# Kernel optimization log

Measured on AMD Instinct MI355X. Metric: run time of the kernel, lower is better.

## Reference

```python
import jax, jax.numpy as jnp
import numpy as np

B, H, W, C = 8, 64, 64, 128
BN_EPS = 1e-3  # keras BatchNormalization default epsilon


def setup_inputs() -> dict:
    key = jax.random.key(0)
    ks = jax.random.split(key, 8)
    scale = 1.0 / np.sqrt(C)
    return {
        "x": jax.random.normal(ks[0], (B, H, W, C), dtype=jnp.float32),
        "wq": jax.random.normal(ks[1], (C, C), dtype=jnp.float32) * scale,
        "bq": jnp.zeros((C,), dtype=jnp.float32),
        "wk": jax.random.normal(ks[2], (C, C), dtype=jnp.float32) * scale,
        "bk": jnp.zeros((C,), dtype=jnp.float32),
        "wv": jax.random.normal(ks[3], (C, C), dtype=jnp.float32) * scale,
        "bv": jnp.zeros((C,), dtype=jnp.float32),
        "gamma": jnp.ones((C,), dtype=jnp.float32),
        "beta": jnp.zeros((C,), dtype=jnp.float32),
        "mov_mean": jax.random.normal(ks[4], (C,), dtype=jnp.float32) * 0.1,
        "mov_var": jax.random.uniform(ks[5], (C,), dtype=jnp.float32) * 0.5 + 0.5,
    }


def reference(x, wq, bq, wk, bk, wv, bv, gamma, beta, mov_mean, mov_var):
    b, h, w, c = x.shape
    n = h * w
    # 1x1 convs == per-pixel linear projections
    q = (jnp.einsum('bhwc,cd->bhwd', x, wq) + bq).reshape(b, n, c)
    k = (jnp.einsum('bhwc,cd->bhwd', x, wk) + bk).reshape(b, n, c)
    v = (jnp.einsum('bhwc,cd->bhwd', x, wv) + bv).reshape(b, n, c)
    # full [n, n] attention matrix (as in the original module)
    scores = jnp.einsum('bnc,bmc->bnm', q, k) / jnp.sqrt(jnp.asarray(c, x.dtype))
    attn = jax.nn.softmax(scores, axis=-1)  # dropout is identity in inference
    out = jnp.einsum('bnm,bmc->bnc', attn, v).reshape(b, h, w, c)
    out = out + x  # residual
    # BatchNormalization, inference mode (moving statistics)
    inv = gamma * jax.lax.rsqrt(mov_var + BN_EPS)
    out = out * inv + (beta - mov_mean * inv)
    return out
```

## Files before the change

kernel.cpp:

```cpp
#include <hip/hip_runtime.h>


typedef __attribute__((ext_vector_type(8))) short bf16x8;
typedef __attribute__((ext_vector_type(4))) float f32x4;

__device__ __forceinline__ unsigned short f2bf(float f) {
  unsigned int u = __builtin_bit_cast(unsigned int, f);
  u += 0x7fffu + ((u >> 16) & 1u);
  return (unsigned short)(u >> 16);
}
__device__ __forceinline__ unsigned int pack2(float a, float b) {
  return (unsigned int)f2bf(a) | ((unsigned int)f2bf(b) << 16);
}

#define SCALE_Q (0.08838834764831845f * 1.44269504088896340f)

__global__ void prep_wt(const float* __restrict__ wq, const float* __restrict__ wk,
                        const float* __restrict__ wv, unsigned short* __restrict__ wt) {
  const float* W = (blockIdx.x == 0) ? wq : (blockIdx.x == 1 ? wk : wv);
  const float sc = (blockIdx.x == 0) ? SCALE_Q : 1.0f;
  unsigned short* out = wt + blockIdx.x * 16384;
  int id = blockIdx.y * 256 + threadIdx.x;
  int n  = id >> 5;
  int kb = (id & 31) * 4;
#pragma unroll
  for (int k = 0; k < 4; ++k)
    out[n * 128 + kb + k] = f2bf(W[(kb + k) * 128 + n] * sc);
}

__global__ __launch_bounds__(256) void qkv_fused(
    const float* __restrict__ x, const unsigned short* __restrict__ wt,
    const float* __restrict__ bq, const float* __restrict__ bk, const float* __restrict__ bv,
    unsigned short* __restrict__ Qg, unsigned short* __restrict__ Kg,
    unsigned short* __restrict__ Vtg) {
  __shared__ unsigned short xs[128 * 128];
  __shared__ unsigned short vlds[128 * 136];
  const int t = threadIdx.x;
  const int rowblk = blockIdx.x * 128;

#pragma unroll
  for (int i = 0; i < 16; ++i) {
    int flat = t * 4 + i * 1024;
    int row = flat >> 7, col = flat & 127;
    float4 v = *(const float4*)(x + (size_t)(rowblk + row) * 128 + col);
    unsigned int u0 = pack2(v.x, v.y), u1 = pack2(v.z, v.w);
    int pos = (col >> 3) ^ (row & 15);
    *(uint2*)(xs + row * 128 + pos * 8 + (col & 7)) = make_uint2(u0, u1);
  }
  __syncthreads();

  const int lane = t & 63, wv_ = t >> 6;
  const int lm = lane & 15, quad = lane >> 4;

  bf16x8 a[2][4];
#pragma unroll
  for (int tr = 0; tr < 2; ++tr) {
    int row = wv_ * 32 + tr * 16 + lm;
#pragma unroll
    for (int ks = 0; ks < 4; ++ks)
      a[tr][ks] = __builtin_bit_cast(bf16x8,
          *(const uint4*)(xs + row * 128 + (((ks * 4 + quad) ^ lm) * 8)));
  }

  const f32x4 zero4 = {0.f, 0.f, 0.f, 0.f};
#pragma unroll 1
  for (int p = 0; p < 3; ++p) {
    const unsigned short* w = wt + p * 16384;
    const float* bias = (p == 0) ? bq : (p == 1 ? bk : bv);
    const float bsc = (p == 0) ? SCALE_Q : 1.0f;

    f32x4 acc[2][8];
#pragma unroll
    for (int tr = 0; tr < 2; ++tr)
#pragma unroll
      for (int ct = 0; ct < 8; ++ct) acc[tr][ct] = zero4;

#pragma unroll
    for (int ct = 0; ct < 8; ++ct) {
      int n = ct * 16 + lm;
      const uint4* wp = (const uint4*)(w + n * 128 + quad * 8);
#pragma unroll
      for (int ks = 0; ks < 4; ++ks) {
        bf16x8 bfr = __builtin_bit_cast(bf16x8, wp[ks * 4]);
        acc[0][ct] = __builtin_amdgcn_mfma_f32_16x16x32_bf16(a[0][ks], bfr, acc[0][ct], 0, 0, 0);
        acc[1][ct] = __builtin_amdgcn_mfma_f32_16x16x32_bf16(a[1][ks], bfr, acc[1][ct], 0, 0, 0);
      }
    }

    if (p < 2) {
      unsigned short* og = (p == 0) ? Qg : Kg;
#pragma unroll
      for (int tr = 0; tr < 2; ++tr) {
        int rowb = rowblk + wv_ * 32 + tr * 16 + quad * 4;
#pragma unroll
        for (int ct = 0; ct < 8; ++ct) {
          int c = ct * 16 + lm;
          float bb = bias[c] * bsc;
#pragma unroll
          for (int r = 0; r < 4; ++r)
            og[(size_t)(rowb + r) * 128 + c] = f2bf(acc[tr][ct][r] + bb);
        }
      }
    } else {
#pragma unroll
      for (int tr = 0; tr < 2; ++tr) {
        int key_base = wv_ * 32 + tr * 16 + quad * 4;
#pragma unroll
        for (int ct = 0; ct < 8; ++ct) {
          int c = ct * 16 + lm;
          float bb = bias[c];
          unsigned int u0 = pack2(acc[tr][ct][0] + bb, acc[tr][ct][1] + bb);
          unsigned int u1 = pack2(acc[tr][ct][2] + bb, acc[tr][ct][3] + bb);
          *(uint2*)(vlds + (size_t)c * 136 + key_base) = make_uint2(u0, u1);
        }
      }
      __syncthreads();
      int c2 = t >> 1;
      int ch = (t & 1) * 8;
      int b  = rowblk >> 12;
      int nb0 = rowblk & 4095;
#pragma unroll
      for (int j = 0; j < 8; ++j) {
        uint4 vv = *(const uint4*)(vlds + (size_t)c2 * 136 + (ch + j) * 8);
        *(uint4*)(Vtg + (size_t)b * 524288 + (size_t)c2 * 4096 + nb0 + (ch + j) * 8) = vv;
      }
    }
  }
}

__global__ __launch_bounds__(256, 2) void flash_attn(
    const unsigned short* __restrict__ Qg, const unsigned short* __restrict__ Kg,
    const unsigned short* __restrict__ Vtg, const float* __restrict__ x,
    const float* __restrict__ gamma, const float* __restrict__ beta,
    const float* __restrict__ mmean, const float* __restrict__ mvar,
    float* __restrict__ out) {
  __shared__ uint4 Pb[2048];
  __shared__ float lred[256];

  const int b  = blockIdx.x & 7;
  const int qt = blockIdx.x >> 3;
  const int t = threadIdx.x;
  const int lane = t & 63;
  const int w = t >> 6;
  const int lm = lane & 15, quad = lane >> 4;
  const int q0 = qt * 64;

  const unsigned short* Qb = Qg  + (size_t)b * 524288;
  const unsigned short* Kb = Kg  + (size_t)b * 524288;
  const unsigned short* Vb = Vtg + (size_t)b * 524288;

  bf16x8 qf[4][4];
#pragma unroll
  for (int nt = 0; nt < 4; ++nt) {
    const uint4* qp = (const uint4*)(Qb + (size_t)(q0 + nt * 16 + lm) * 128 + quad * 8);
#pragma unroll
    for (int ks = 0; ks < 4; ++ks) qf[nt][ks] = __builtin_bit_cast(bf16x8, qp[ks * 4]);
  }

  const f32x4 zero4 = {0.f, 0.f, 0.f, 0.f};
  f32x4 o[2][4];
#pragma unroll
  for (int mt = 0; mt < 2; ++mt)
#pragma unroll
    for (int nt = 0; nt < 4; ++nt) o[mt][nt] = zero4;
  float lp[4] = {0.f, 0.f, 0.f, 0.f};

  for (int kt = 0; kt < 32; ++kt) {
    const int key0 = kt * 128;

    bf16x8 kf[2][4], vf[2][4];
#pragma unroll
    for (int mt = 0; mt < 2; ++mt) {
      const uint4* kp = (const uint4*)(Kb + (size_t)(key0 + w * 32 + mt * 16 + lm) * 128 + quad * 8);
      const uint4* vp = (const uint4*)(Vb + (size_t)(w * 32 + mt * 16 + lm) * 4096 + key0 + quad * 8);
#pragma unroll
      for (int ks = 0; ks < 4; ++ks) {
        kf[mt][ks] = __builtin_bit_cast(bf16x8, kp[ks * 4]);
        vf[mt][ks] = __builtin_bit_cast(bf16x8, vp[ks * 4]);
      }
    }

    f32x4 sa[2][4];
#pragma unroll
    for (int mt = 0; mt < 2; ++mt)
#pragma unroll
      for (int nt = 0; nt < 4; ++nt) sa[mt][nt] = zero4;
#pragma unroll
    for (int ks = 0; ks < 4; ++ks)
#pragma unroll
      for (int mt = 0; mt < 2; ++mt)
#pragma unroll
        for (int nt = 0; nt < 4; ++nt)
          sa[mt][nt] = __builtin_amdgcn_mfma_f32_16x16x32_bf16(kf[mt][ks], qf[nt][ks], sa[mt][nt], 0, 0, 0);

    unsigned short* Ps = (unsigned short*)(Pb + (kt & 1) * 1024);
    const int sub = (quad & 1) * 4;
#pragma unroll
    for (int mt = 0; mt < 2; ++mt) {
      int c16 = w * 4 + mt * 2 + (quad >> 1);
      int pos = c16 ^ lm;
#pragma unroll
      for (int nt = 0; nt < 4; ++nt) {
        float e0 = exp2f(sa[mt][nt][0]), e1 = exp2f(sa[mt][nt][1]);
        float e2 = exp2f(sa[mt][nt][2]), e3 = exp2f(sa[mt][nt][3]);
        lp[nt] += (e0 + e1) + (e2 + e3);
        *(uint2*)(Ps + (nt * 16 + lm) * 128 + pos * 8 + sub) =
            make_uint2(pack2(e0, e1), pack2(e2, e3));
      }
    }
    __syncthreads();

    const uint4* Pr = Pb + (kt & 1) * 1024;
#pragma unroll
    for (int nt = 0; nt < 4; ++nt) {
      bf16x8 pf[4];
#pragma unroll
      for (int ks = 0; ks < 4; ++ks)
        pf[ks] = __builtin_bit_cast(bf16x8, Pr[(nt * 16 + lm) * 16 + ((ks * 4 + quad) ^ lm)]);
#pragma unroll
      for (int ks = 0; ks < 4; ++ks)
#pragma unroll
        for (int mt = 0; mt < 2; ++mt)
          o[mt][nt] = __builtin_amdgcn_mfma_f32_16x16x32_bf16(vf[mt][ks], pf[ks], o[mt][nt], 0, 0, 0);
    }
  }

#pragma unroll
  for (int nt = 0; nt < 4; ++nt) {
    lp[nt] += __shfl_xor(lp[nt], 16);
    lp[nt] += __shfl_xor(lp[nt], 32);
  }
  if (quad == 0) {
#pragma unroll
    for (int nt = 0; nt < 4; ++nt) lred[w * 64 + nt * 16 + lm] = lp[nt];
  }
  __syncthreads();
  float rl[4];
#pragma unroll
  for (int nt = 0; nt < 4; ++nt) {
    int q = nt * 16 + lm;
    rl[nt] = 1.0f / ((lred[q] + lred[64 + q]) + (lred[128 + q] + lred[192 + q]));
  }

#pragma unroll
  for (int mt = 0; mt < 2; ++mt) {
    int c0 = w * 32 + mt * 16 + quad * 4;
    float4 gm = *(const float4*)(gamma + c0);
    float4 bt = *(const float4*)(beta + c0);
    float4 mm = *(const float4*)(mmean + c0);
    float4 mv = *(const float4*)(mvar + c0);
    float iv0 = gm.x * rsqrtf(mv.x + 1e-3f), iv1 = gm.y * rsqrtf(mv.y + 1e-3f);
    float iv2 = gm.z * rsqrtf(mv.z + 1e-3f), iv3 = gm.w * rsqrtf(mv.w + 1e-3f);
    float ad0 = bt.x - mm.x * iv0, ad1 = bt.y - mm.y * iv1;
    float ad2 = bt.z - mm.z * iv2, ad3 = bt.w - mm.w * iv3;
#pragma unroll
    for (int nt = 0; nt < 4; ++nt) {
      size_t g = ((size_t)b * 4096 + q0 + nt * 16 + lm) * 128 + c0;
      float4 xr = *(const float4*)(x + g);
      float4 ov;
      ov.x = (o[mt][nt][0] * rl[nt] + xr.x) * iv0 + ad0;
      ov.y = (o[mt][nt][1] * rl[nt] + xr.y) * iv1 + ad1;
      ov.z = (o[mt][nt][2] * rl[nt] + xr.z) * iv2 + ad2;
      ov.w = (o[mt][nt][3] * rl[nt] + xr.w) * iv3 + ad3;
      *(float4*)(out + g) = ov;
    }
  }
}

extern "C" void kernel_launch(void* const* d_in, const int* in_sizes, int n_in,
                              void* d_out, int out_size, void* d_ws, size_t ws_size,
                              hipStream_t stream) {
  const float* x     = (const float*)d_in[0];
  const float* wq    = (const float*)d_in[1];
  const float* bq    = (const float*)d_in[2];
  const float* wk    = (const float*)d_in[3];
  const float* bk    = (const float*)d_in[4];
  const float* wv    = (const float*)d_in[5];
  const float* bv    = (const float*)d_in[6];
  const float* gamma = (const float*)d_in[7];
  const float* beta  = (const float*)d_in[8];
  const float* mmean = (const float*)d_in[9];
  const float* mvar  = (const float*)d_in[10];
  float* out = (float*)d_out;

  unsigned short* wt  = (unsigned short*)d_ws;
  unsigned short* Qg  = wt + 3 * 128 * 128;
  unsigned short* Kg  = Qg + 8 * 4096 * 128;
  unsigned short* Vtg = Kg + 8 * 4096 * 128;

  prep_wt<<<dim3(3, 16), dim3(256), 0, stream>>>(wq, wk, wv, wt);
  qkv_fused<<<dim3(256), dim3(256), 0, stream>>>(x, wt, bq, bk, bv, Qg, Kg, Vtg);
  flash_attn<<<dim3(512), dim3(256), 0, stream>>>(Qg, Kg, Vtg, x, gamma, beta, mmean, mvar, out);
}
```

Before: 233.4 us.

## Prefetch next K tile in attention loop and stage Q/K stores through LDS

The attention loop is restructured to double-buffer the K fragments: the next tile's K is loaded into registers while the current tile is processed, with a manual two-step unroll. This aims to hide global load latency behind the MFMA work. Separately, the QKV projection now stages Q and K outputs through a shared LDS buffer, so global writes become coalesced 16-byte stores instead of scattered 2-byte ones, at the cost of two extra barriers per projection. The extra K registers may lower occupancy under the launch bounds.

```diff
diff --git a/kernel.cpp b/kernel.cpp
--- a/kernel.cpp
+++ b/kernel.cpp
@@ -34,7 +34,7 @@
     unsigned short* __restrict__ Qg, unsigned short* __restrict__ Kg,
     unsigned short* __restrict__ Vtg) {
   __shared__ unsigned short xs[128 * 128];
-  __shared__ unsigned short vlds[128 * 136];
+  __shared__ unsigned short obuf[128 * 136];
   const int t = threadIdx.x;
   const int rowblk = blockIdx.x * 128;
 
@@ -63,6 +63,11 @@
   }
 
   const f32x4 zero4 = {0.f, 0.f, 0.f, 0.f};
+  const int b   = rowblk >> 12;
+  const int nb0 = rowblk & 4095;
+  const int rrow = t >> 1;
+  const int rch  = (t & 1) * 8;
+
 #pragma unroll 1
   for (int p = 0; p < 3; ++p) {
     const unsigned short* w = wt + p * 16384;
@@ -88,19 +93,26 @@
     }
 
     if (p < 2) {
-      unsigned short* og = (p == 0) ? Qg : Kg;
 #pragma unroll
       for (int tr = 0; tr < 2; ++tr) {
-        int rowb = rowblk + wv_ * 32 + tr * 16 + quad * 4;
+        int rowb = wv_ * 32 + tr * 16 + quad * 4;
 #pragma unroll
         for (int ct = 0; ct < 8; ++ct) {
           int c = ct * 16 + lm;
           float bb = bias[c] * bsc;
 #pragma unroll
           for (int r = 0; r < 4; ++r)
-            og[(size_t)(rowb + r) * 128 + c] = f2bf(acc[tr][ct][r] + bb);
+            obuf[(rowb + r) * 136 + c] = f2bf(acc[tr][ct][r] + bb);
         }
       }
+      __syncthreads();
+      unsigned short* og = (p == 0) ? Qg : Kg;
+#pragma unroll
+      for (int j = 0; j < 8; ++j) {
+        uint4 vv = *(const uint4*)(obuf + rrow * 136 + (rch + j) * 8);
+        *(uint4*)(og + (size_t)(rowblk + rrow) * 128 + (rch + j) * 8) = vv;
+      }
+      __syncthreads();
     } else {
 #pragma unroll
       for (int tr = 0; tr < 2; ++tr) {
@@ -111,18 +123,14 @@
           float bb = bias[c];
           unsigned int u0 = pack2(acc[tr][ct][0] + bb, acc[tr][ct][1] + bb);
           unsigned int u1 = pack2(acc[tr][ct][2] + bb, acc[tr][ct][3] + bb);
-          *(uint2*)(vlds + (size_t)c * 136 + key_base) = make_uint2(u0, u1);
+          *(uint2*)(obuf + (size_t)c * 136 + key_base) = make_uint2(u0, u1);
         }
       }
       __syncthreads();
-      int c2 = t >> 1;
-      int ch = (t & 1) * 8;
-      int b  = rowblk >> 12;
-      int nb0 = rowblk & 4095;
 #pragma unroll
       for (int j = 0; j < 8; ++j) {
-        uint4 vv = *(const uint4*)(vlds + (size_t)c2 * 136 + (ch + j) * 8);
-        *(uint4*)(Vtg + (size_t)b * 524288 + (size_t)c2 * 4096 + nb0 + (ch + j) * 8) = vv;
+        uint4 vv = *(const uint4*)(obuf + rrow * 136 + (rch + j) * 8);
+        *(uint4*)(Vtg + (size_t)b * 524288 + (size_t)rrow * 4096 + nb0 + (rch + j) * 8) = vv;
       }
     }
   }
@@ -165,21 +173,28 @@
     for (int nt = 0; nt < 4; ++nt) o[mt][nt] = zero4;
   float lp[4] = {0.f, 0.f, 0.f, 0.f};
 
-  for (int kt = 0; kt < 32; ++kt) {
+  bf16x8 kf0[2][4], kf1[2][4];
+
+  auto loadK = [&](int kt, bf16x8 (&kf)[2][4]) {
     const int key0 = kt * 128;
-
-    bf16x8 kf[2][4], vf[2][4];
 #pragma unroll
     for (int mt = 0; mt < 2; ++mt) {
       const uint4* kp = (const uint4*)(Kb + (size_t)(key0 + w * 32 + mt * 16 + lm) * 128 + quad * 8);
+#pragma unroll
+      for (int ks = 0; ks < 4; ++ks) kf[mt][ks] = __builtin_bit_cast(bf16x8, kp[ks * 4]);
+    }
+  };
+  auto loadV = [&](int kt, bf16x8 (&vf)[2][4]) {
+    const int key0 = kt * 128;
+#pragma unroll
+    for (int mt = 0; mt < 2; ++mt) {
       const uint4* vp = (const uint4*)(Vb + (size_t)(w * 32 + mt * 16 + lm) * 4096 + key0 + quad * 8);
 #pragma unroll
-      for (int ks = 0; ks < 4; ++ks) {
-        kf[mt][ks] = __builtin_bit_cast(bf16x8, kp[ks * 4]);
-        vf[mt][ks] = __builtin_bit_cast(bf16x8, vp[ks * 4]);
-      }
-    }
-
+      for (int ks = 0; ks < 4; ++ks) vf[mt][ks] = __builtin_bit_cast(bf16x8, vp[ks * 4]);
+    }
+  };
+
+  auto body = [&](int kt, bf16x8 (&kf)[2][4], bf16x8 (&vf)[2][4]) {
     f32x4 sa[2][4];
 #pragma unroll
     for (int mt = 0; mt < 2; ++mt)
@@ -222,6 +237,23 @@
 #pragma unroll
         for (int mt = 0; mt < 2; ++mt)
           o[mt][nt] = __builtin_amdgcn_mfma_f32_16x16x32_bf16(vf[mt][ks], pf[ks], o[mt][nt], 0, 0, 0);
+    }
+  };
+
+  loadK(0, kf0);
+#pragma unroll 1
+  for (int kt = 0; kt < 32; kt += 2) {
+    {
+      bf16x8 vf[2][4];
+      loadV(kt, vf);
+      loadK(kt + 1, kf1);
+      body(kt, kf0, vf);
+    }
+    {
+      bf16x8 vf[2][4];
+      loadV(kt + 1, vf);
+      if (kt + 2 < 32) loadK(kt + 2, kf0);
+      body(kt + 1, kf1, vf);
     }
   }
 
```

After: 254.5 us. 1.09x slower.

## Split attention over key halves with combine kernel and finer QKV grid

Applied to the files above, without the earlier changes.

The QKV projection kernel now launches one block per 64-row tile per projection (512x3 grid) and stages Q/K outputs through shared memory for coalesced 16-byte stores. The attention kernel can split each query tile's keys into two halves, writing partial unnormalized outputs and row sums to workspace, and a new combine kernel merges them and applies the residual and batchnorm. The split doubles the attention grid (1024 blocks) and raises the occupancy hint to 4 blocks per CU, so the work fills more of the GPU. In exchange it adds an extra kernel launch and about 32 MB of fp32 partial-output traffic. The split path is taken only when the workspace is large enough.

```diff
diff --git a/kernel.cpp b/kernel.cpp
--- a/kernel.cpp
+++ b/kernel.cpp
@@ -28,18 +28,19 @@
     out[n * 128 + kb + k] = f2bf(W[(kb + k) * 128 + n] * sc);
 }
 
-__global__ __launch_bounds__(256) void qkv_fused(
+__global__ __launch_bounds__(256) void qkv_proj(
     const float* __restrict__ x, const unsigned short* __restrict__ wt,
     const float* __restrict__ bq, const float* __restrict__ bk, const float* __restrict__ bv,
     unsigned short* __restrict__ Qg, unsigned short* __restrict__ Kg,
     unsigned short* __restrict__ Vtg) {
-  __shared__ unsigned short xs[128 * 128];
-  __shared__ unsigned short vlds[128 * 136];
+  __shared__ unsigned short xs[64 * 128];
+  __shared__ unsigned short obuf[9216];
   const int t = threadIdx.x;
-  const int rowblk = blockIdx.x * 128;
-
-#pragma unroll
-  for (int i = 0; i < 16; ++i) {
+  const int p = blockIdx.y;
+  const int rowblk = blockIdx.x * 64;
+
+#pragma unroll
+  for (int i = 0; i < 8; ++i) {
     int flat = t * 4 + i * 1024;
     int row = flat >> 7, col = flat & 127;
     float4 v = *(const float4*)(x + (size_t)(rowblk + row) * 128 + col);
@@ -52,93 +53,99 @@
   const int lane = t & 63, wv_ = t >> 6;
   const int lm = lane & 15, quad = lane >> 4;
 
-  bf16x8 a[2][4];
-#pragma unroll
-  for (int tr = 0; tr < 2; ++tr) {
-    int row = wv_ * 32 + tr * 16 + lm;
+  bf16x8 a[4];
+  {
+    int row = wv_ * 16 + lm;
 #pragma unroll
     for (int ks = 0; ks < 4; ++ks)
-      a[tr][ks] = __builtin_bit_cast(bf16x8,
+      a[ks] = __builtin_bit_cast(bf16x8,
           *(const uint4*)(xs + row * 128 + (((ks * 4 + quad) ^ lm) * 8)));
   }
 
+  const unsigned short* w = wt + p * 16384;
+  const float* bias = (p == 0) ? bq : (p == 1 ? bk : bv);
+  const float bsc = (p == 0) ? SCALE_Q : 1.0f;
+
   const f32x4 zero4 = {0.f, 0.f, 0.f, 0.f};
-#pragma unroll 1
-  for (int p = 0; p < 3; ++p) {
-    const unsigned short* w = wt + p * 16384;
-    const float* bias = (p == 0) ? bq : (p == 1 ? bk : bv);
-    const float bsc = (p == 0) ? SCALE_Q : 1.0f;
-
-    f32x4 acc[2][8];
-#pragma unroll
-    for (int tr = 0; tr < 2; ++tr)
-#pragma unroll
-      for (int ct = 0; ct < 8; ++ct) acc[tr][ct] = zero4;
-
+  f32x4 acc[8];
+#pragma unroll
+  for (int ct = 0; ct < 8; ++ct) acc[ct] = zero4;
+
+#pragma unroll
+  for (int ct = 0; ct < 8; ++ct) {
+    int n = ct * 16 + lm;
+    const uint4* wp = (const uint4*)(w + n * 128 + quad * 8);
+#pragma unroll
+    for (int ks = 0; ks < 4; ++ks) {
+      bf16x8 bfr = __builtin_bit_cast(bf16x8, wp[ks * 4]);
+      acc[ct] = __builtin_amdgcn_mfma_f32_16x16x32_bf16(a[ks], bfr, acc[ct], 0, 0, 0);
+    }
+  }
+
+  const int b   = rowblk >> 12;
+  const int nb0 = rowblk & 4095;
+
+  if (p < 2) {
+    int rowb = wv_ * 16 + quad * 4;
 #pragma unroll
     for (int ct = 0; ct < 8; ++ct) {
-      int n = ct * 16 + lm;
-      const uint4* wp = (const uint4*)(w + n * 128 + quad * 8);
-#pragma unroll
-      for (int ks = 0; ks < 4; ++ks) {
-        bf16x8 bfr = __builtin_bit_cast(bf16x8, wp[ks * 4]);
-        acc[0][ct] = __builtin_amdgcn_mfma_f32_16x16x32_bf16(a[0][ks], bfr, acc[0][ct], 0, 0, 0);
-        acc[1][ct] = __builtin_amdgcn_mfma_f32_16x16x32_bf16(a[1][ks], bfr, acc[1][ct], 0, 0, 0);
-      }
-    }
-
-    if (p < 2) {
-      unsigned short* og = (p == 0) ? Qg : Kg;
-#pragma unroll
-      for (int tr = 0; tr < 2; ++tr) {
-        int rowb = rowblk + wv_ * 32 + tr * 16 + quad * 4;
-#pragma unroll
-        for (int ct = 0; ct < 8; ++ct) {
-          int c = ct * 16 + lm;
-          float bb = bias[c] * bsc;
-#pragma unroll
-          for (int r = 0; r < 4; ++r)
-            og[(size_t)(rowb + r) * 128 + c] = f2bf(acc[tr][ct][r] + bb);
-        }
-      }
-    } else {
-#pragma unroll
-      for (int tr = 0; tr < 2; ++tr) {
-        int key_base = wv_ * 32 + tr * 16 + quad * 4;
-#pragma unroll
-        for (int ct = 0; ct < 8; ++ct) {
-          int c = ct * 16 + lm;
-          float bb = bias[c];
-          unsigned int u0 = pack2(acc[tr][ct][0] + bb, acc[tr][ct][1] + bb);
-          unsigned int u1 = pack2(acc[tr][ct][2] + bb, acc[tr][ct][3] + bb);
-          *(uint2*)(vlds + (size_t)c * 136 + key_base) = make_uint2(u0, u1);
-        }
-      }
-      __syncthreads();
-      int c2 = t >> 1;
-      int ch = (t & 1) * 8;
-      int b  = rowblk >> 12;
-      int nb0 = rowblk & 4095;
-#pragma unroll
-      for (int j = 0; j < 8; ++j) {
-        uint4 vv = *(const uint4*)(vlds + (size_t)c2 * 136 + (ch + j) * 8);
-        *(uint4*)(Vtg + (size_t)b * 524288 + (size_t)c2 * 4096 + nb0 + (ch + j) * 8) = vv;
-      }
-    }
-  }
-}
-
-__global__ __launch_bounds__(256, 2) void flash_attn(
+      int c = ct * 16 + lm;
+      float bb = bias[c] * bsc;
+#pragma unroll
+      for (int r = 0; r < 4; ++r)
+        obuf[(rowb + r) * 136 + c] = f2bf(acc[ct][r] + bb);
+    }
+    __syncthreads();
+    unsigned short* og = (p == 0) ? Qg : Kg;
+    int row = t >> 2;
+#pragma unroll
+    for (int j = 0; j < 4; ++j) {
+      int ch = (t & 3) * 4 + j;
+      uint4 vv = *(const uint4*)(obuf + row * 136 + ch * 8);
+      *(uint4*)(og + (size_t)(rowblk + row) * 128 + ch * 8) = vv;
+    }
+  } else {
+    int key_base = wv_ * 16 + quad * 4;
+#pragma unroll
+    for (int ct = 0; ct < 8; ++ct) {
+      int c = ct * 16 + lm;
+      float bb = bias[c];
+      unsigned int u0 = pack2(acc[ct][0] + bb, acc[ct][1] + bb);
+      unsigned int u1 = pack2(acc[ct][2] + bb, acc[ct][3] + bb);
+      *(uint2*)(obuf + c * 72 + key_base) = make_uint2(u0, u1);
+    }
+    __syncthreads();
+    int d = t >> 1;
+#pragma unroll
+    for (int j = 0; j < 4; ++j) {
+      int ch = (t & 1) * 4 + j;
+      uint4 vv = *(const uint4*)(obuf + d * 72 + ch * 8);
+      *(uint4*)(Vtg + (size_t)b * 524288 + (size_t)d * 4096 + nb0 + ch * 8) = vv;
+    }
+  }
+}
+
+__global__ __launch_bounds__(256, 4) void flash_attn(
     const unsigned short* __restrict__ Qg, const unsigned short* __restrict__ Kg,
     const unsigned short* __restrict__ Vtg, const float* __restrict__ x,
     const float* __restrict__ gamma, const float* __restrict__ beta,
     const float* __restrict__ mmean, const float* __restrict__ mvar,
-    float* __restrict__ out) {
+    float* __restrict__ out, float* __restrict__ Ow, float* __restrict__ lw,
+    int split) {
   __shared__ uint4 Pb[2048];
   __shared__ float lred[256];
 
-  const int b  = blockIdx.x & 7;
-  const int qt = blockIdx.x >> 3;
+  const int b = blockIdx.x & 7;
+  int qt, kt0, ktn, slot;
+  if (split) {
+    qt  = blockIdx.x >> 4;
+    int kh = (blockIdx.x >> 3) & 1;
+    kt0 = kh * 16; ktn = 16;
+    slot = (b * 64 + qt) * 2 + kh;
+  } else {
+    qt = blockIdx.x >> 3;
+    kt0 = 0; ktn = 32; slot = 0;
+  }
   const int t = threadIdx.x;
   const int lane = t & 63;
   const int w = t >> 6;
@@ -165,8 +172,9 @@
     for (int nt = 0; nt < 4; ++nt) o[mt][nt] = zero4;
   float lp[4] = {0.f, 0.f, 0.f, 0.f};
 
-  for (int kt = 0; kt < 32; ++kt) {
-    const int key0 = kt * 128;
+#pragma unroll 1
+  for (int kti = 0; kti < ktn; ++kti) {
+    const int key0 = (kt0 + kti) * 128;
 
     bf16x8 kf[2][4], vf[2][4];
 #pragma unroll
@@ -193,7 +201,7 @@
         for (int nt = 0; nt < 4; ++nt)
           sa[mt][nt] = __builtin_amdgcn_mfma_f32_16x16x32_bf16(kf[mt][ks], qf[nt][ks], sa[mt][nt], 0, 0, 0);
 
-    unsigned short* Ps = (unsigned short*)(Pb + (kt & 1) * 1024);
+    unsigned short* Ps = (unsigned short*)(Pb + (kti & 1) * 1024);
     const int sub = (quad & 1) * 4;
 #pragma unroll
     for (int mt = 0; mt < 2; ++mt) {
@@ -210,7 +218,7 @@
     }
     __syncthreads();
 
-    const uint4* Pr = Pb + (kt & 1) * 1024;
+    const uint4* Pr = Pb + (kti & 1) * 1024;
 #pragma unroll
     for (int nt = 0; nt < 4; ++nt) {
       bf16x8 pf[4];
@@ -235,6 +243,25 @@
     for (int nt = 0; nt < 4; ++nt) lred[w * 64 + nt * 16 + lm] = lp[nt];
   }
   __syncthreads();
+
+  if (split) {
+    if (t < 64)
+      lw[slot * 64 + t] = (lred[t] + lred[64 + t]) + (lred[128 + t] + lred[192 + t]);
+    float* Op = Ow + (size_t)slot * 8192;
+#pragma unroll
+    for (int mt = 0; mt < 2; ++mt) {
+      int c0 = w * 32 + mt * 16 + quad * 4;
+#pragma unroll
+      for (int nt = 0; nt < 4; ++nt) {
+        float4 ov;
+        ov.x = o[mt][nt][0]; ov.y = o[mt][nt][1];
+        ov.z = o[mt][nt][2]; ov.w = o[mt][nt][3];
+        *(float4*)(Op + (nt * 16 + lm) * 128 + c0) = ov;
+      }
+    }
+    return;
+  }
+
   float rl[4];
 #pragma unroll
   for (int nt = 0; nt < 4; ++nt) {
@@ -265,6 +292,40 @@
       *(float4*)(out + g) = ov;
     }
   }
+}
+
+__global__ __launch_bounds__(256) void combine(
+    const float* __restrict__ Ow, const float* __restrict__ lw,
+    const float* __restrict__ x,
+    const float* __restrict__ gamma, const float* __restrict__ beta,
+    const float* __restrict__ mmean, const float* __restrict__ mvar,
+    float* __restrict__ out) {
+  int flat4 = blockIdx.x * 256 + threadIdx.x;
+  int g  = flat4 * 4;
+  int row = g >> 7;
+  int c0  = g & 127;
+  int bq = row >> 12;
+  int n  = row & 4095;
+  int qt = n >> 6, qq = n & 63;
+  int slot = (bq * 64 + qt) * 2;
+
+  float l = lw[slot * 64 + qq] + lw[(slot + 1) * 64 + qq];
+  float rl = 1.0f / l;
+  float4 O0 = *(const float4*)(Ow + (size_t)slot * 8192 + qq * 128 + c0);
+  float4 O1 = *(const float4*)(Ow + (size_t)(slot + 1) * 8192 + qq * 128 + c0);
+  float4 gm = *(const float4*)(gamma + c0);
+  float4 bt = *(const float4*)(beta + c0);
+  float4 mm = *(const float4*)(mmean + c0);
+  float4 mv = *(const float4*)(mvar + c0);
+  float iv0 = gm.x * rsqrtf(mv.x + 1e-3f), iv1 = gm.y * rsqrtf(mv.y + 1e-3f);
+  float iv2 = gm.z * rsqrtf(mv.z + 1e-3f), iv3 = gm.w * rsqrtf(mv.w + 1e-3f);
+  float4 xr = *(const float4*)(x + g);
+  float4 ov;
+  ov.x = ((O0.x + O1.x) * rl + xr.x) * iv0 + (bt.x - mm.x * iv0);
+  ov.y = ((O0.y + O1.y) * rl + xr.y) * iv1 + (bt.y - mm.y * iv1);
+  ov.z = ((O0.z + O1.z) * rl + xr.z) * iv2 + (bt.z - mm.z * iv2);
+  ov.w = ((O0.w + O1.w) * rl + xr.w) * iv3 + (bt.w - mm.w * iv3);
+  *(float4*)(out + g) = ov;
 }
 
 extern "C" void kernel_launch(void* const* d_in, const int* in_sizes, int n_in,
@@ -287,8 +348,20 @@
   unsigned short* Qg  = wt + 3 * 128 * 128;
   unsigned short* Kg  = Qg + 8 * 4096 * 128;
   unsigned short* Vtg = Kg + 8 * 4096 * 128;
+  float* Ow = (float*)(Vtg + 8 * 4096 * 128);
+  float* lw = Ow + 1024 * 8192;
+
+  const size_t need = 98304ull + 3ull * 8388608ull + 33554432ull + 262144ull;
+  const int split = (ws_size >= need) ? 1 : 0;
 
   prep_wt<<<dim3(3, 16), dim3(256), 0, stream>>>(wq, wk, wv, wt);
-  qkv_fused<<<dim3(256), dim3(256), 0, stream>>>(x, wt, bq, bk, bv, Qg, Kg, Vtg);
-  flash_attn<<<dim3(512), dim3(256), 0, stream>>>(Qg, Kg, Vtg, x, gamma, beta, mmean, mvar, out);
-}
+  qkv_proj<<<dim3(512, 3), dim3(256), 0, stream>>>(x, wt, bq, bk, bv, Qg, Kg, Vtg);
+  if (split) {
+    flash_attn<<<dim3(1024), dim3(256), 0, stream>>>(Qg, Kg, Vtg, x, gamma, beta,
+                                                     mmean, mvar, out, Ow, lw, 1);
+    combine<<<dim3(4096), dim3(256), 0, stream>>>(Ow, lw, x, gamma, beta, mmean, mvar, out);
+  } else {
+    flash_attn<<<dim3(512), dim3(256), 0, stream>>>(Qg, Kg, Vtg, x, gamma, beta,
+                                                    mmean, mvar, out, Ow, lw, 0);
+  }
+}
```

Result: slower. 371.9 us (+59.3%).

## Split QKV projection across grid and widen attention blocks to 8 waves

Applied to the files above, without the earlier changes.

The QKV projection now launches one block per 64-row tile and per projection (Q, K or V) in a 512x3 grid, instead of looping over all three projections on 128-row tiles. Q and K outputs are staged through LDS so they can be written with coalesced 16-byte stores. The attention kernel moves from 4 to 8 waves per block: each wave handles 16 queries against 64 keys for the scores and 16 value channels for the output, so per-wave register use drops and latency hiding improves. In exchange, x is loaded and staged three times in the projection, and each attention wave now re-reads the K tiles for its key half.

```diff
diff --git a/kernel.cpp b/kernel.cpp
--- a/kernel.cpp
+++ b/kernel.cpp
@@ -28,18 +28,19 @@
     out[n * 128 + kb + k] = f2bf(W[(kb + k) * 128 + n] * sc);
 }
 
-__global__ __launch_bounds__(256) void qkv_fused(
+__global__ __launch_bounds__(256) void qkv_proj(
     const float* __restrict__ x, const unsigned short* __restrict__ wt,
     const float* __restrict__ bq, const float* __restrict__ bk, const float* __restrict__ bv,
     unsigned short* __restrict__ Qg, unsigned short* __restrict__ Kg,
     unsigned short* __restrict__ Vtg) {
-  __shared__ unsigned short xs[128 * 128];
-  __shared__ unsigned short vlds[128 * 136];
+  __shared__ unsigned short xs[64 * 128];
+  __shared__ unsigned short obuf[9216];
   const int t = threadIdx.x;
-  const int rowblk = blockIdx.x * 128;
-
-#pragma unroll
-  for (int i = 0; i < 16; ++i) {
+  const int p = blockIdx.y;
+  const int rowblk = blockIdx.x * 64;
+
+#pragma unroll
+  for (int i = 0; i < 8; ++i) {
     int flat = t * 4 + i * 1024;
     int row = flat >> 7, col = flat & 127;
     float4 v = *(const float4*)(x + (size_t)(rowblk + row) * 128 + col);
@@ -52,96 +53,94 @@
   const int lane = t & 63, wv_ = t >> 6;
   const int lm = lane & 15, quad = lane >> 4;
 
-  bf16x8 a[2][4];
-#pragma unroll
-  for (int tr = 0; tr < 2; ++tr) {
-    int row = wv_ * 32 + tr * 16 + lm;
+  bf16x8 a[4];
+  {
+    int row = wv_ * 16 + lm;
 #pragma unroll
     for (int ks = 0; ks < 4; ++ks)
-      a[tr][ks] = __builtin_bit_cast(bf16x8,
+      a[ks] = __builtin_bit_cast(bf16x8,
           *(const uint4*)(xs + row * 128 + (((ks * 4 + quad) ^ lm) * 8)));
   }
 
+  const unsigned short* w = wt + p * 16384;
+  const float* bias = (p == 0) ? bq : (p == 1 ? bk : bv);
+  const float bsc = (p == 0) ? SCALE_Q : 1.0f;
+
   const f32x4 zero4 = {0.f, 0.f, 0.f, 0.f};
-#pragma unroll 1
-  for (int p = 0; p < 3; ++p) {
-    const unsigned short* w = wt + p * 16384;
-    const float* bias = (p == 0) ? bq : (p == 1 ? bk : bv);
-    const float bsc = (p == 0) ? SCALE_Q : 1.0f;
-
-    f32x4 acc[2][8];
-#pragma unroll
-    for (int tr = 0; tr < 2; ++tr)
-#pragma unroll
-      for (int ct = 0; ct < 8; ++ct) acc[tr][ct] = zero4;
-
+  f32x4 acc[8];
+#pragma unroll
+  for (int ct = 0; ct < 8; ++ct) acc[ct] = zero4;
+
+#pragma unroll
+  for (int ct = 0; ct < 8; ++ct) {
+    int n = ct * 16 + lm;
+    const uint4* wp = (const uint4*)(w + n * 128 + quad * 8);
+#pragma unroll
+    for (int ks = 0; ks < 4; ++ks) {
+      bf16x8 bfr = __builtin_bit_cast(bf16x8, wp[ks * 4]);
+      acc[ct] = __builtin_amdgcn_mfma_f32_16x16x32_bf16(a[ks], bfr, acc[ct], 0, 0, 0);
+    }
+  }
+
+  const int b   = rowblk >> 12;
+  const int nb0 = rowblk & 4095;
+
+  if (p < 2) {
+    int rowb = wv_ * 16 + quad * 4;
 #pragma unroll
     for (int ct = 0; ct < 8; ++ct) {
-      int n = ct * 16 + lm;
-      const uint4* wp = (const uint4*)(w + n * 128 + quad * 8);
-#pragma unroll
-      for (int ks = 0; ks < 4; ++ks) {
-        bf16x8 bfr = __builtin_bit_cast(bf16x8, wp[ks * 4]);
-        acc[0][ct] = __builtin_amdgcn_mfma_f32_16x16x32_bf16(a[0][ks], bfr, acc[0][ct], 0, 0, 0);
-        acc[1][ct] = __builtin_amdgcn_mfma_f32_16x16x32_bf16(a[1][ks], bfr, acc[1][ct], 0, 0, 0);
-      }
-    }
-
-    if (p < 2) {
-      unsigned short* og = (p == 0) ? Qg : Kg;
-#pragma unroll
-      for (int tr = 0; tr < 2; ++tr) {
-        int rowb = rowblk + wv_ * 32 + tr * 16 + quad * 4;
-#pragma unroll
-        for (int ct = 0; ct < 8; ++ct) {
-          int c = ct * 16 + lm;
-          float bb = bias[c] * bsc;
-#pragma unroll
-          for (int r = 0; r < 4; ++r)
-            og[(size_t)(rowb + r) * 128 + c] = f2bf(acc[tr][ct][r] + bb);
-        }
-      }
-    } else {
-#pragma unroll
-      for (int tr = 0; tr < 2; ++tr) {
-        int key_base = wv_ * 32 + tr * 16 + quad * 4;
-#pragma unroll
-        for (int ct = 0; ct < 8; ++ct) {
-          int c = ct * 16 + lm;
-          float bb = bias[c];
-          unsigned int u0 = pack2(acc[tr][ct][0] + bb, acc[tr][ct][1] + bb);
-          unsigned int u1 = pack2(acc[tr][ct][2] + bb, acc[tr][ct][3] + bb);
-          *(uint2*)(vlds + (size_t)c * 136 + key_base) = make_uint2(u0, u1);
-        }
-      }
-      __syncthreads();
-      int c2 = t >> 1;
-      int ch = (t & 1) * 8;
-      int b  = rowblk >> 12;
-      int nb0 = rowblk & 4095;
-#pragma unroll
-      for (int j = 0; j < 8; ++j) {
-        uint4 vv = *(const uint4*)(vlds + (size_t)c2 * 136 + (ch + j) * 8);
-        *(uint4*)(Vtg + (size_t)b * 524288 + (size_t)c2 * 4096 + nb0 + (ch + j) * 8) = vv;
-      }
-    }
-  }
-}
-
-__global__ __launch_bounds__(256, 2) void flash_attn(
+      int c = ct * 16 + lm;
+      float bb = bias[c] * bsc;
+#pragma unroll
+      for (int r = 0; r < 4; ++r)
+        obuf[(rowb + r) * 136 + c] = f2bf(acc[ct][r] + bb);
+    }
+    __syncthreads();
+    unsigned short* og = (p == 0) ? Qg : Kg;
+    int row = t >> 2;
+#pragma unroll
+    for (int j = 0; j < 4; ++j) {
+      int ch = (t & 3) * 4 + j;
+      uint4 vv = *(const uint4*)(obuf + row * 136 + ch * 8);
+      *(uint4*)(og + (size_t)(rowblk + row) * 128 + ch * 8) = vv;
+    }
+  } else {
+    int key_base = wv_ * 16 + quad * 4;
+#pragma unroll
+    for (int ct = 0; ct < 8; ++ct) {
+      int c = ct * 16 + lm;
+      float bb = bias[c];
+      unsigned int u0 = pack2(acc[ct][0] + bb, acc[ct][1] + bb);
+      unsigned int u1 = pack2(acc[ct][2] + bb, acc[ct][3] + bb);
+      *(uint2*)(obuf + c * 72 + key_base) = make_uint2(u0, u1);
+    }
+    __syncthreads();
+    int d = t >> 1;
+#pragma unroll
+    for (int j = 0; j < 4; ++j) {
+      int ch = (t & 1) * 4 + j;
+      uint4 vv = *(const uint4*)(obuf + d * 72 + ch * 8);
+      *(uint4*)(Vtg + (size_t)b * 524288 + (size_t)d * 4096 + nb0 + ch * 8) = vv;
+    }
+  }
+}
+
+__global__ __launch_bounds__(512, 2) void flash_attn(
     const unsigned short* __restrict__ Qg, const unsigned short* __restrict__ Kg,
     const unsigned short* __restrict__ Vtg, const float* __restrict__ x,
     const float* __restrict__ gamma, const float* __restrict__ beta,
     const float* __restrict__ mmean, const float* __restrict__ mvar,
     float* __restrict__ out) {
   __shared__ uint4 Pb[2048];
-  __shared__ float lred[256];
+  __shared__ float lred[128];
 
   const int b  = blockIdx.x & 7;
   const int qt = blockIdx.x >> 3;
   const int t = threadIdx.x;
   const int lane = t & 63;
   const int w = t >> 6;
+  const int kw = w & 1;
+  const int qw = w >> 1;
   const int lm = lane & 15, quad = lane >> 4;
   const int q0 = qt * 64;
 
@@ -149,64 +148,56 @@
   const unsigned short* Kb = Kg  + (size_t)b * 524288;
   const unsigned short* Vb = Vtg + (size_t)b * 524288;
 
-  bf16x8 qf[4][4];
-#pragma unroll
-  for (int nt = 0; nt < 4; ++nt) {
-    const uint4* qp = (const uint4*)(Qb + (size_t)(q0 + nt * 16 + lm) * 128 + quad * 8);
-#pragma unroll
-    for (int ks = 0; ks < 4; ++ks) qf[nt][ks] = __builtin_bit_cast(bf16x8, qp[ks * 4]);
+  bf16x8 qf[4];
+  {
+    const uint4* qp = (const uint4*)(Qb + (size_t)(q0 + qw * 16 + lm) * 128 + quad * 8);
+#pragma unroll
+    for (int ks = 0; ks < 4; ++ks) qf[ks] = __builtin_bit_cast(bf16x8, qp[ks * 4]);
   }
 
   const f32x4 zero4 = {0.f, 0.f, 0.f, 0.f};
-  f32x4 o[2][4];
-#pragma unroll
-  for (int mt = 0; mt < 2; ++mt)
-#pragma unroll
-    for (int nt = 0; nt < 4; ++nt) o[mt][nt] = zero4;
-  float lp[4] = {0.f, 0.f, 0.f, 0.f};
-
+  f32x4 o[4];
+#pragma unroll
+  for (int nt = 0; nt < 4; ++nt) o[nt] = zero4;
+  float lp = 0.f;
+
+#pragma unroll 1
   for (int kt = 0; kt < 32; ++kt) {
     const int key0 = kt * 128;
 
-    bf16x8 kf[2][4], vf[2][4];
-#pragma unroll
-    for (int mt = 0; mt < 2; ++mt) {
-      const uint4* kp = (const uint4*)(Kb + (size_t)(key0 + w * 32 + mt * 16 + lm) * 128 + quad * 8);
-      const uint4* vp = (const uint4*)(Vb + (size_t)(w * 32 + mt * 16 + lm) * 4096 + key0 + quad * 8);
-#pragma unroll
-      for (int ks = 0; ks < 4; ++ks) {
-        kf[mt][ks] = __builtin_bit_cast(bf16x8, kp[ks * 4]);
-        vf[mt][ks] = __builtin_bit_cast(bf16x8, vp[ks * 4]);
-      }
-    }
-
-    f32x4 sa[2][4];
-#pragma unroll
-    for (int mt = 0; mt < 2; ++mt)
-#pragma unroll
-      for (int nt = 0; nt < 4; ++nt) sa[mt][nt] = zero4;
-#pragma unroll
-    for (int ks = 0; ks < 4; ++ks)
-#pragma unroll
-      for (int mt = 0; mt < 2; ++mt)
-#pragma unroll
-        for (int nt = 0; nt < 4; ++nt)
-          sa[mt][nt] = __builtin_amdgcn_mfma_f32_16x16x32_bf16(kf[mt][ks], qf[nt][ks], sa[mt][nt], 0, 0, 0);
+    bf16x8 vf[4];
+    {
+      const uint4* vp = (const uint4*)(Vb + (size_t)(w * 16 + lm) * 4096 + key0 + quad * 8);
+#pragma unroll
+      for (int ks = 0; ks < 4; ++ks) vf[ks] = __builtin_bit_cast(bf16x8, vp[ks * 4]);
+    }
+
+    f32x4 sa[4];
+#pragma unroll
+    for (int mt = 0; mt < 4; ++mt) sa[mt] = zero4;
+#pragma unroll
+    for (int mt = 0; mt < 4; ++mt) {
+      const uint4* kp = (const uint4*)(Kb + (size_t)(key0 + kw * 64 + mt * 16 + lm) * 128 + quad * 8);
+      bf16x8 kf[4];
+#pragma unroll
+      for (int ks = 0; ks < 4; ++ks) kf[ks] = __builtin_bit_cast(bf16x8, kp[ks * 4]);
+#pragma unroll
+      for (int ks = 0; ks < 4; ++ks)
+        sa[mt] = __builtin_amdgcn_mfma_f32_16x16x32_bf16(kf[ks], qf[ks], sa[mt], 0, 0, 0);
+    }
 
     unsigned short* Ps = (unsigned short*)(Pb + (kt & 1) * 1024);
     const int sub = (quad & 1) * 4;
-#pragma unroll
-    for (int mt = 0; mt < 2; ++mt) {
-      int c16 = w * 4 + mt * 2 + (quad >> 1);
+    const int prow = qw * 16 + lm;
+#pragma unroll
+    for (int mt = 0; mt < 4; ++mt) {
+      int c16 = kw * 8 + mt * 2 + (quad >> 1);
       int pos = c16 ^ lm;
-#pragma unroll
-      for (int nt = 0; nt < 4; ++nt) {
-        float e0 = exp2f(sa[mt][nt][0]), e1 = exp2f(sa[mt][nt][1]);
-        float e2 = exp2f(sa[mt][nt][2]), e3 = exp2f(sa[mt][nt][3]);
-        lp[nt] += (e0 + e1) + (e2 + e3);
-        *(uint2*)(Ps + (nt * 16 + lm) * 128 + pos * 8 + sub) =
-            make_uint2(pack2(e0, e1), pack2(e2, e3));
-      }
+      float e0 = exp2f(sa[mt][0]), e1 = exp2f(sa[mt][1]);
+      float e2 = exp2f(sa[mt][2]), e3 = exp2f(sa[mt][3]);
+      lp += (e0 + e1) + (e2 + e3);
+      *(uint2*)(Ps + prow * 128 + pos * 8 + sub) =
+          make_uint2(pack2(e0, e1), pack2(e2, e3));
     }
     __syncthreads();
 
@@ -219,32 +210,21 @@
         pf[ks] = __builtin_bit_cast(bf16x8, Pr[(nt * 16 + lm) * 16 + ((ks * 4 + quad) ^ lm)]);
 #pragma unroll
       for (int ks = 0; ks < 4; ++ks)
-#pragma unroll
-        for (int mt = 0; mt < 2; ++mt)
-          o[mt][nt] = __builtin_amdgcn_mfma_f32_16x16x32_bf16(vf[mt][ks], pf[ks], o[mt][nt], 0, 0, 0);
-    }
-  }
-
-#pragma unroll
-  for (int nt = 0; nt < 4; ++nt) {
-    lp[nt] += __shfl_xor(lp[nt], 16);
-    lp[nt] += __shfl_xor(lp[nt], 32);
-  }
-  if (quad == 0) {
-#pragma unroll
-    for (int nt = 0; nt < 4; ++nt) lred[w * 64 + nt * 16 + lm] = lp[nt];
-  }
+        o[nt] = __builtin_amdgcn_mfma_f32_16x16x32_bf16(vf[ks], pf[ks], o[nt], 0, 0, 0);
+    }
+  }
+
+  lp += __shfl_xor(lp, 16);
+  lp += __shfl_xor(lp, 32);
+  if (quad == 0) lred[(qw * 2 + kw) * 16 + lm] = lp;
   __syncthreads();
   float rl[4];
 #pragma unroll
-  for (int nt = 0; nt < 4; ++nt) {
-    int q = nt * 16 + lm;
-    rl[nt] = 1.0f / ((lred[q] + lred[64 + q]) + (lred[128 + q] + lred[192 + q]));
-  }
-
-#pragma unroll
-  for (int mt = 0; mt < 2; ++mt) {
-    int c0 = w * 32 + mt * 16 + quad * 4;
+  for (int nt = 0; nt < 4; ++nt)
+    rl[nt] = 1.0f / (lred[nt * 32 + lm] + lred[nt * 32 + 16 + lm]);
+
+  {
+    int c0 = w * 16 + quad * 4;
     float4 gm = *(const float4*)(gamma + c0);
     float4 bt = *(const float4*)(beta + c0);
     float4 mm = *(const float4*)(mmean + c0);
@@ -258,10 +238,10 @@
       size_t g = ((size_t)b * 4096 + q0 + nt * 16 + lm) * 128 + c0;
       float4 xr = *(const float4*)(x + g);
       float4 ov;
-      ov.x = (o[mt][nt][0] * rl[nt] + xr.x) * iv0 + ad0;
-      ov.y = (o[mt][nt][1] * rl[nt] + xr.y) * iv1 + ad1;
-      ov.z = (o[mt][nt][2] * rl[nt] + xr.z) * iv2 + ad2;
-      ov.w = (o[mt][nt][3] * rl[nt] + xr.w) * iv3 + ad3;
+      ov.x = (o[nt][0] * rl[nt] + xr.x) * iv0 + ad0;
+      ov.y = (o[nt][1] * rl[nt] + xr.y) * iv1 + ad1;
+      ov.z = (o[nt][2] * rl[nt] + xr.z) * iv2 + ad2;
+      ov.w = (o[nt][3] * rl[nt] + xr.w) * iv3 + ad3;
       *(float4*)(out + g) = ov;
     }
   }
@@ -289,6 +269,7 @@
   unsigned short* Vtg = Kg + 8 * 4096 * 128;
 
   prep_wt<<<dim3(3, 16), dim3(256), 0, stream>>>(wq, wk, wv, wt);
-  qkv_fused<<<dim3(256), dim3(256), 0, stream>>>(x, wt, bq, bk, bv, Qg, Kg, Vtg);
-  flash_attn<<<dim3(512), dim3(256), 0, stream>>>(Qg, Kg, Vtg, x, gamma, beta, mmean, mvar, out);
-}
+  qkv_proj<<<dim3(512, 3), dim3(256), 0, stream>>>(x, wt, bq, bk, bv, Qg, Kg, Vtg);
+  flash_attn<<<dim3(512), dim3(512), 0, stream>>>(Qg, Kg, Vtg, x, gamma, beta,
+                                                  mmean, mvar, out);
+}
```

Result: slower. 409.0 us (+75.2%).
